# Kernel tuning notes

Measured on AMD Instinct MI355X. Metric: run time of the kernel, lower is better.

## Reference

```python
import jax, jax.numpy as jnp
import numpy as np

B, S, H = 4, 2048, 4096   # batch, seq, hidden
Q_DIM = 32 * 128          # num_attention_heads * head_dim
KV_DIM = 8 * 128          # num_key_value_heads * head_dim
R = 16                    # lora_r
SCALING = 32.0 / 16.0     # lora_alpha / lora_r


def setup_inputs() -> dict:
    key = jax.random.key(0)
    ks = jax.random.split(key, 10)
    def n(k, shape, scale):
        return jax.random.normal(k, shape, dtype=jnp.float32) * scale
    x = jax.random.normal(ks[0], (B, S, H), dtype=jnp.float32)
    # base weights stored as [out_dim, in_dim] like nn.Linear
    Wq = n(ks[1], (Q_DIM, H), 0.02)
    Wk = n(ks[2], (KV_DIM, H), 0.02)
    Wv = n(ks[3], (KV_DIM, H), 0.02)
    bq = n(ks[4], (Q_DIM,), 0.02)
    bk = n(ks[5], (KV_DIM,), 0.02)
    bv = n(ks[6], (KV_DIM,), 0.02)
    # LoRA A: kaiming-uniform-like init; B: zeros in training start, use small
    # random values here so the LoRA path is numerically exercised.
    bound = 1.0 / np.sqrt(H)
    Aq = jax.random.uniform(ks[7], (H, R), jnp.float32, -bound, bound)
    Ak = jax.random.uniform(ks[8], (H, R), jnp.float32, -bound, bound)
    Av = jax.random.uniform(ks[9], (H, R), jnp.float32, -bound, bound)
    kb = jax.random.split(jax.random.fold_in(key, 1), 3)
    Bq = n(kb[0], (R, Q_DIM), 0.01)
    Bk = n(kb[1], (R, KV_DIM), 0.01)
    Bv = n(kb[2], (R, KV_DIM), 0.01)
    return {"x": x, "Wq": Wq, "Wk": Wk, "Wv": Wv, "bq": bq, "bk": bk, "bv": bv,
            "Aq": Aq, "Bq": Bq, "Ak": Ak, "Bk": Bk, "Av": Av, "Bv": Bv}


def _proj(x, W, b, A, Bm):
    # base GEMM + low-rank LoRA delta + bias (dropout p=0 -> identity)
    base = jnp.einsum('bsh,oh->bso', x, W)
    delta = jnp.einsum('bsr,ro->bso', jnp.einsum('bsh,hr->bsr', x, A), Bm)
    return base + SCALING * delta + b


def reference(x, Wq, Wk, Wv, bq, bk, bv, Aq, Bq, Ak, Bk, Av, Bv):
    q = _proj(x, Wq, bq, Aq, Bq)  # [B,S,Q_DIM]
    k = _proj(x, Wk, bk, Ak, Bk)  # [B,S,KV_DIM]
    v = _proj(x, Wv, bv, Av, Bv)  # [B,S,KV_DIM]
    return q, k, v
```

## Files before the change

kernel.cpp:

```cpp
#include <hip/hip_runtime.h>


#define GLOBAL_AS __attribute__((address_space(1)))
#define LDS_AS    __attribute__((address_space(3)))

typedef __attribute__((ext_vector_type(8))) short  short8;
typedef __attribute__((ext_vector_type(4))) float  floatx4;

constexpr int Mdim = 8192;
constexpr int Kdim = 4096;
constexpr int NQ   = 4096;
constexpr int NKV  = 1024;
constexpr int NTOT = NQ + 2 * NKV;
constexpr float LORA_SCALE = 2.0f;

constexpr int BM = 256, BN = 256;
constexpr int TILES_M = Mdim / BM;
constexpr int TILES_N = NTOT / BN;
constexpr int NWG = TILES_M * TILES_N;
constexpr int NSLICE = Kdim / 32;

constexpr int WEFF_BLOCKS = (NTOT / 64) * (Kdim / 512);
constexpr int CVT_BLOCKS  = 2048;
constexpr int AT_STRIDE   = 516;

__device__ __forceinline__ unsigned short f2bf(float f) {
    union { float f; unsigned int u; } a; a.f = f;
    unsigned int r = a.u + 0x7FFFu + ((a.u >> 16) & 1u);
    return (unsigned short)(r >> 16);
}

__global__ __launch_bounds__(256)
void prep_kernel(const float4* __restrict__ x4, unsigned short* __restrict__ Xbf,
                 const float* __restrict__ Wq, const float* __restrict__ Wk,
                 const float* __restrict__ Wv,
                 const float* __restrict__ Aq, const float* __restrict__ Bq,
                 const float* __restrict__ Ak, const float* __restrict__ Bk,
                 const float* __restrict__ Av, const float* __restrict__ Bv,
                 unsigned short* __restrict__ Wf) {
    __shared__ float AsT[16 * AT_STRIDE];
    __shared__ float Bsc[64 * 16];

    const int tid = threadIdx.x;

    if (blockIdx.x >= WEFF_BLOCKS) {
        int i = (blockIdx.x - WEFF_BLOCKS) * 256 + tid;
        const int stride = CVT_BLOCKS * 256;
        const int n4 = Mdim * Kdim / 4;
        ushort4* out = (ushort4*)Xbf;
        for (; i < n4; i += stride) {
            float4 v = x4[i];
            ushort4 u;
            u.x = f2bf(v.x); u.y = f2bf(v.y); u.z = f2bf(v.z); u.w = f2bf(v.w);
            out[i] = u;
        }
        return;
    }

    const int n0 = (blockIdx.x >> 3) * 64;
    const int h0 = (blockIdx.x & 7) * 512;

    const float* W; const float* A; const float* Bm; int O; int nn0;
    if (n0 < NQ)            { W = Wq; A = Aq; Bm = Bq; O = NQ;  nn0 = n0; }
    else if (n0 < NQ + NKV) { W = Wk; A = Ak; Bm = Bk; O = NKV; nn0 = n0 - NQ; }
    else                    { W = Wv; A = Av; Bm = Bv; O = NKV; nn0 = n0 - NQ - NKV; }

    {
        const float4* Af4 = (const float4*)(A) + h0 * 4;
        #pragma unroll
        for (int i = 0; i < 8; ++i) {
            const int f = i * 256 + tid;
            const float4 v = Af4[f];
            const int hl = f >> 2;
            const int r0 = (f & 3) * 4;
            AsT[(r0 + 0) * AT_STRIDE + hl] = v.x;
            AsT[(r0 + 1) * AT_STRIDE + hl] = v.y;
            AsT[(r0 + 2) * AT_STRIDE + hl] = v.z;
            AsT[(r0 + 3) * AT_STRIDE + hl] = v.w;
        }
    }
    {
        const int nl = tid & 63;
        const int rq = tid >> 6;
        #pragma unroll
        for (int j = 0; j < 4; ++j) {
            const int r = rq * 4 + j;
            Bsc[nl * 16 + r] = Bm[r * O + nn0 + nl] * LORA_SCALE;
        }
    }
    __syncthreads();

    const int wv_ = tid >> 6;
    const int lane = tid & 63;

    #pragma unroll
    for (int pass = 0; pass < 2; ++pass) {
        const int hl = pass * 256 + lane * 4;
        float4 areg[16];
        #pragma unroll
        for (int r = 0; r < 16; ++r)
            areg[r] = *(const float4*)(&AsT[r * AT_STRIDE + hl]);

        for (int i = 0; i < 16; ++i) {
            const int nl = wv_ * 16 + i;
            const float4 w4 = *(const float4*)(W + (size_t)(nn0 + nl) * Kdim + h0 + hl);
            const float4* b4 = (const float4*)(&Bsc[nl * 16]);
            float4 d = {0.f, 0.f, 0.f, 0.f};
            #pragma unroll
            for (int q = 0; q < 4; ++q) {
                const float4 b = b4[q];
                d.x += areg[q*4+0].x * b.x + areg[q*4+1].x * b.y + areg[q*4+2].x * b.z + areg[q*4+3].x * b.w;
                d.y += areg[q*4+0].y * b.x + areg[q*4+1].y * b.y + areg[q*4+2].y * b.z + areg[q*4+3].y * b.w;
                d.z += areg[q*4+0].z * b.x + areg[q*4+1].z * b.y + areg[q*4+2].z * b.z + areg[q*4+3].z * b.w;
                d.w += areg[q*4+0].w * b.x + areg[q*4+1].w * b.y + areg[q*4+2].w * b.z + areg[q*4+3].w * b.w;
            }
            ushort4 u;
            u.x = f2bf(w4.x + d.x); u.y = f2bf(w4.y + d.y);
            u.z = f2bf(w4.z + d.z); u.w = f2bf(w4.w + d.w);
            *(ushort4*)(Wf + (size_t)(n0 + nl) * Kdim + h0 + hl) = u;
        }
    }
}

__global__ __launch_bounds__(512, 2)
void gemm_qkv_kernel(const unsigned short* __restrict__ X,
                     const unsigned short* __restrict__ Wf,
                     const float* __restrict__ bq, const float* __restrict__ bk,
                     const float* __restrict__ bv,
                     float* __restrict__ out) {
    __shared__ __align__(16) unsigned short Abuf[4][8192];
    __shared__ __align__(16) unsigned short Bbuf[4][8192];

    const int tid  = threadIdx.x;
    const int lane = tid & 63;
    const int w    = tid >> 6;
    const int wr   = w >> 2;
    const int wc   = w & 3;

    int bid = blockIdx.x;
    bid = (bid & 7) * (NWG / 8) + (bid >> 3);
    const int row0 = (bid / TILES_N) * BM;
    const int col0 = (bid % TILES_N) * BN;

    const int swz    = (((lane >> 4) ^ ((lane >> 1) & 3)) << 4);
    const int aByte0 = (wr * 128 + (lane & 15)) * 64 + swz;
    const int bByte0 = (wc * 64  + (lane & 15)) * 64 + swz;

    const int srow = (w << 4) + (lane >> 2);
    const int kswz = (((lane & 3) ^ ((lane >> 3) & 3)) << 3);
    const unsigned short* pA0 = X  + (size_t)(row0 + srow) * Kdim + kswz;
    const unsigned short* pA1 = pA0 + (size_t)128 * Kdim;
    const unsigned short* pB0 = Wf + (size_t)(col0 + srow) * Kdim + kswz;
    const unsigned short* pB1 = pB0 + (size_t)128 * Kdim;

    floatx4 acc[8][4];
    #pragma unroll
    for (int i = 0; i < 8; ++i)
        #pragma unroll
        for (int j = 0; j < 4; ++j)
            acc[i][j] = (floatx4){0.f, 0.f, 0.f, 0.f};

    short8 afr[2][4];
    short8 bfr[2][4];

#define STAGE(MATA, SS, SLOT)                                                    \
    { const int ss_ = (SS);                                                      \
      if (MATA) {                                                                \
        __builtin_amdgcn_global_load_lds((const GLOBAL_AS void*)(pA0 + ss_ * 32),\
            (LDS_AS void*)(&Abuf[SLOT][w * 512]),        16, 0, 0);              \
        __builtin_amdgcn_global_load_lds((const GLOBAL_AS void*)(pA1 + ss_ * 32),\
            (LDS_AS void*)(&Abuf[SLOT][4096 + w * 512]), 16, 0, 0);              \
      } else {                                                                   \
        __builtin_amdgcn_global_load_lds((const GLOBAL_AS void*)(pB0 + ss_ * 32),\
            (LDS_AS void*)(&Bbuf[SLOT][w * 512]),        16, 0, 0);              \
        __builtin_amdgcn_global_load_lds((const GLOBAL_AS void*)(pB1 + ss_ * 32),\
            (LDS_AS void*)(&Bbuf[SLOT][4096 + w * 512]), 16, 0, 0);              \
      } }

#define READA(P, SLOT, MH)                                                       \
    { const char* ab_ = (const char*)Abuf + (SLOT) * 16384;                      \
      _Pragma("unroll")                                                          \
      for (int mf = 0; mf < 4; ++mf)                                             \
        afr[P][mf] = *(const short8*)(ab_ + aByte0 + ((MH) * 4 + mf) * 1024); }

#define READB(P, SLOT)                                                           \
    { const char* bb_ = (const char*)Bbuf + (SLOT) * 16384;                      \
      _Pragma("unroll")                                                          \
      for (int nf = 0; nf < 4; ++nf)                                             \
        bfr[P][nf] = *(const short8*)(bb_ + bByte0 + nf * 1024); }

#define MFMA16(PA, PB, MH)                                                       \
    { __builtin_amdgcn_s_setprio(1);                                             \
      _Pragma("unroll")                                                          \
      for (int mf = 0; mf < 4; ++mf)                                             \
        _Pragma("unroll")                                                        \
        for (int nf = 0; nf < 4; ++nf)                                           \
          acc[(MH) * 4 + mf][nf] = __builtin_amdgcn_mfma_f32_16x16x32_bf16(      \
              afr[PA][mf], bfr[PB][nf], acc[(MH) * 4 + mf][nf], 0, 0, 0);        \
      __builtin_amdgcn_s_setprio(0); }

#define PHASE(PAC, PBC, MH, PRA, NAP, NSLOT, NMH, PRB, NBP, DOST, SM, SS, SSLOT, WM, BAR) \
    { if (PRA) READA(NAP, NSLOT, NMH);                                           \
      if (PRB) READB(NBP, NSLOT);                                                \
      if (DOST) STAGE(SM, SS, SSLOT);                                            \
      MFMA16(PAC, PBC, MH);                                                      \
      if ((WM) == 1) asm volatile("s_waitcnt vmcnt(6)" ::: "memory");            \
      if ((WM) == 2) asm volatile("s_waitcnt vmcnt(4)" ::: "memory");            \
      if ((WM) == 3) asm volatile("s_waitcnt vmcnt(0)" ::: "memory");            \
      if (BAR) __builtin_amdgcn_s_barrier(); }

    STAGE(1, 0, 0); STAGE(0, 0, 0);
    STAGE(1, 1, 1); STAGE(0, 1, 1);
    STAGE(1, 2, 2); STAGE(0, 2, 2);
    asm volatile("s_waitcnt vmcnt(8)" ::: "memory");
    __builtin_amdgcn_s_barrier();
    READA(0, 0, 0);
    READB(0, 0);

    for (int j = 0; j < NSLICE / 4 - 1; ++j) {
        const int g = j * 4;
        PHASE(0,  0,  0,  1,  1,  0,    1,  0,  0,   1,   1,  g + 3, 3,    1, 1);
        PHASE(1,  0,  1,  1,  0,  1,    0,  1,  1,   1,   0,  g + 3, 3,    0, 1);
        PHASE(0,  1,  0,  1,  1,  1,    1,  0,  0,   1,   1,  g + 4, 0,    1, 1);
        PHASE(1,  1,  1,  1,  0,  2,    0,  1,  0,   1,   0,  g + 4, 0,    0, 1);
        PHASE(0,  0,  0,  1,  1,  2,    1,  0,  0,   1,   1,  g + 5, 1,    1, 1);
        PHASE(1,  0,  1,  1,  0,  3,    0,  1,  1,   1,   0,  g + 5, 1,    0, 1);
        PHASE(0,  1,  0,  1,  1,  3,    1,  0,  0,   1,   1,  g + 6, 2,    1, 1);
        PHASE(1,  1,  1,  1,  0,  0,    0,  1,  0,   1,   0,  g + 6, 2,    0, 1);
    }
    PHASE(0, 0, 0,  1, 1, 0, 1,  0, 0,  1, 1, 127, 3,  1, 1);
    PHASE(1, 0, 1,  1, 0, 1, 0,  1, 1,  1, 0, 127, 3,  0, 1);
    PHASE(0, 1, 0,  1, 1, 1, 1,  0, 0,  0, 0, 0,   0,  2, 1);
    PHASE(1, 1, 1,  1, 0, 2, 0,  1, 0,  0, 0, 0,   0,  0, 1);
    PHASE(0, 0, 0,  1, 1, 2, 1,  0, 0,  0, 0, 0,   0,  3, 1);
    PHASE(1, 0, 1,  1, 0, 3, 0,  1, 1,  0, 0, 0,   0,  0, 1);
    PHASE(0, 1, 0,  1, 1, 3, 1,  0, 0,  0, 0, 0,   0,  0, 1);
    PHASE(1, 1, 1,  0, 0, 0, 0,  0, 0,  0, 0, 0,   0,  0, 0);

#undef PHASE
#undef MFMA16
#undef READB
#undef READA
#undef STAGE

    float* obase; int ldo; const float* bias; int cofs;
    if (col0 < NQ) {
        obase = out;                             ldo = NQ;  bias = bq; cofs = 0;
    } else if (col0 < NQ + NKV) {
        obase = out + (size_t)Mdim * NQ;         ldo = NKV; bias = bk; cofs = NQ;
    } else {
        obase = out + (size_t)Mdim * (NQ + NKV); ldo = NKV; bias = bv; cofs = NQ + NKV;
    }

    #pragma unroll
    for (int nf = 0; nf < 4; ++nf) {
        const int col = col0 + wc * 64 + nf * 16 + (lane & 15) - cofs;
        const float b = bias[col];
        #pragma unroll
        for (int mf = 0; mf < 8; ++mf) {
            #pragma unroll
            for (int r = 0; r < 4; ++r) {
                const int row = row0 + wr * 128 + mf * 16 + (lane >> 4) * 4 + r;
                obase[(size_t)row * ldo + col] = acc[mf][nf][r] + b;
            }
        }
    }
}

extern "C" void kernel_launch(void* const* d_in, const int* in_sizes, int n_in,
                              void* d_out, int out_size, void* d_ws, size_t ws_size,
                              hipStream_t stream) {
    const float* x  = (const float*)d_in[0];
    const float* Wq = (const float*)d_in[1];
    const float* Wk = (const float*)d_in[2];
    const float* Wv = (const float*)d_in[3];
    const float* bq = (const float*)d_in[4];
    const float* bk = (const float*)d_in[5];
    const float* bv = (const float*)d_in[6];
    const float* Aq = (const float*)d_in[7];
    const float* Bq = (const float*)d_in[8];
    const float* Ak = (const float*)d_in[9];
    const float* Bk = (const float*)d_in[10];
    const float* Av = (const float*)d_in[11];
    const float* Bv = (const float*)d_in[12];
    float* out = (float*)d_out;

    unsigned short* Xbf = (unsigned short*)d_ws;
    unsigned short* Wf  = Xbf + (size_t)Mdim * Kdim;

    prep_kernel<<<WEFF_BLOCKS + CVT_BLOCKS, 256, 0, stream>>>(
        (const float4*)x, Xbf, Wq, Wk, Wv, Aq, Bq, Ak, Bk, Av, Bv, Wf);

    gemm_qkv_kernel<<<NWG, 512, 0, stream>>>(Xbf, Wf, bq, bk, bv, out);
}
```

Baseline: 472.9 us.

## Restructure GEMM main loop into per-slice phases with unswizzled LDS layout

```diff
diff --git a/kernel.cpp b/kernel.cpp
--- a/kernel.cpp
+++ b/kernel.cpp
@@ -142,15 +142,15 @@
     const int row0 = (bid / TILES_N) * BM;
     const int col0 = (bid % TILES_N) * BN;
 
-    const int swz    = (((lane >> 4) ^ ((lane >> 1) & 3)) << 4);
-    const int aByte0 = (wr * 128 + (lane & 15)) * 64 + swz;
-    const int bByte0 = (wc * 64  + (lane & 15)) * 64 + swz;
-
-    const int srow = (w << 4) + (lane >> 2);
-    const int kswz = (((lane & 3) ^ ((lane >> 3) & 3)) << 3);
-    const unsigned short* pA0 = X  + (size_t)(row0 + srow) * Kdim + kswz;
+    const int lane16 = lane * 16;
+    const int aBase0 = wr * 8192 + lane16;
+    const int bBase0 = (wc >> 1) * 8192 + (wc & 1) * 4096 + lane16;
+
+    const int srow = w * 16 + (lane & 15);
+    const int kofs = (lane >> 4) * 8;
+    const unsigned short* pA0 = X  + (size_t)(row0 + srow) * Kdim + kofs;
     const unsigned short* pA1 = pA0 + (size_t)128 * Kdim;
-    const unsigned short* pB0 = Wf + (size_t)(col0 + srow) * Kdim + kswz;
+    const unsigned short* pB0 = Wf + (size_t)(col0 + srow) * Kdim + kofs;
     const unsigned short* pB1 = pB0 + (size_t)128 * Kdim;
 
     floatx4 acc[8][4];
@@ -160,88 +160,63 @@
         for (int j = 0; j < 4; ++j)
             acc[i][j] = (floatx4){0.f, 0.f, 0.f, 0.f};
 
-    short8 afr[2][4];
-    short8 bfr[2][4];
-
-#define STAGE(MATA, SS, SLOT)                                                    \
+#define STAGE4(SS, SLOT)                                                         \
     { const int ss_ = (SS);                                                      \
-      if (MATA) {                                                                \
-        __builtin_amdgcn_global_load_lds((const GLOBAL_AS void*)(pA0 + ss_ * 32),\
-            (LDS_AS void*)(&Abuf[SLOT][w * 512]),        16, 0, 0);              \
-        __builtin_amdgcn_global_load_lds((const GLOBAL_AS void*)(pA1 + ss_ * 32),\
-            (LDS_AS void*)(&Abuf[SLOT][4096 + w * 512]), 16, 0, 0);              \
-      } else {                                                                   \
-        __builtin_amdgcn_global_load_lds((const GLOBAL_AS void*)(pB0 + ss_ * 32),\
-            (LDS_AS void*)(&Bbuf[SLOT][w * 512]),        16, 0, 0);              \
-        __builtin_amdgcn_global_load_lds((const GLOBAL_AS void*)(pB1 + ss_ * 32),\
-            (LDS_AS void*)(&Bbuf[SLOT][4096 + w * 512]), 16, 0, 0);              \
-      } }
-
-#define READA(P, SLOT, MH)                                                       \
-    { const char* ab_ = (const char*)Abuf + (SLOT) * 16384;                      \
+      __builtin_amdgcn_global_load_lds((const GLOBAL_AS void*)(pA0 + ss_ * 32),  \
+          (LDS_AS void*)(&Abuf[SLOT][w * 512]),        16, 0, 0);                \
+      __builtin_amdgcn_global_load_lds((const GLOBAL_AS void*)(pA1 + ss_ * 32),  \
+          (LDS_AS void*)(&Abuf[SLOT][4096 + w * 512]), 16, 0, 0);                \
+      __builtin_amdgcn_global_load_lds((const GLOBAL_AS void*)(pB0 + ss_ * 32),  \
+          (LDS_AS void*)(&Bbuf[SLOT][w * 512]),        16, 0, 0);                \
+      __builtin_amdgcn_global_load_lds((const GLOBAL_AS void*)(pB1 + ss_ * 32),  \
+          (LDS_AS void*)(&Bbuf[SLOT][4096 + w * 512]), 16, 0, 0); }
+
+#define SLICE_PHASE(SLOT, DOSTAGE, SS, WM)                                       \
+    { const char* ab_ = (const char*)Abuf + (SLOT) * 16384 + aBase0;             \
+      const char* bb_ = (const char*)Bbuf + (SLOT) * 16384 + bBase0;             \
+      short8 af[8]; short8 bfr[4];                                               \
       _Pragma("unroll")                                                          \
-      for (int mf = 0; mf < 4; ++mf)                                             \
-        afr[P][mf] = *(const short8*)(ab_ + aByte0 + ((MH) * 4 + mf) * 1024); }
-
-#define READB(P, SLOT)                                                           \
-    { const char* bb_ = (const char*)Bbuf + (SLOT) * 16384;                      \
+      for (int mf = 0; mf < 8; ++mf)                                             \
+        af[mf] = *(const short8*)(ab_ + mf * 1024);                              \
       _Pragma("unroll")                                                          \
       for (int nf = 0; nf < 4; ++nf)                                             \
-        bfr[P][nf] = *(const short8*)(bb_ + bByte0 + nf * 1024); }
-
-#define MFMA16(PA, PB, MH)                                                       \
-    { __builtin_amdgcn_s_setprio(1);                                             \
+        bfr[nf] = *(const short8*)(bb_ + nf * 1024);                             \
+      if (DOSTAGE) STAGE4(SS, (SS) & 3);                                         \
+      __builtin_amdgcn_s_barrier();                                              \
+      asm volatile("s_waitcnt lgkmcnt(0)");                                      \
+      __builtin_amdgcn_s_setprio(1);                                             \
       _Pragma("unroll")                                                          \
-      for (int mf = 0; mf < 4; ++mf)                                             \
+      for (int mf = 0; mf < 8; ++mf)                                             \
         _Pragma("unroll")                                                        \
         for (int nf = 0; nf < 4; ++nf)                                           \
-          acc[(MH) * 4 + mf][nf] = __builtin_amdgcn_mfma_f32_16x16x32_bf16(      \
-              afr[PA][mf], bfr[PB][nf], acc[(MH) * 4 + mf][nf], 0, 0, 0);        \
-      __builtin_amdgcn_s_setprio(0); }
-
-#define PHASE(PAC, PBC, MH, PRA, NAP, NSLOT, NMH, PRB, NBP, DOST, SM, SS, SSLOT, WM, BAR) \
-    { if (PRA) READA(NAP, NSLOT, NMH);                                           \
-      if (PRB) READB(NBP, NSLOT);                                                \
-      if (DOST) STAGE(SM, SS, SSLOT);                                            \
-      MFMA16(PAC, PBC, MH);                                                      \
-      if ((WM) == 1) asm volatile("s_waitcnt vmcnt(6)" ::: "memory");            \
+          acc[mf][nf] = __builtin_amdgcn_mfma_f32_16x16x32_bf16(                 \
+              af[mf], bfr[nf], acc[mf][nf], 0, 0, 0);                            \
+      __builtin_amdgcn_s_setprio(0);                                             \
+      if ((WM) == 1) asm volatile("s_waitcnt vmcnt(8)" ::: "memory");            \
       if ((WM) == 2) asm volatile("s_waitcnt vmcnt(4)" ::: "memory");            \
       if ((WM) == 3) asm volatile("s_waitcnt vmcnt(0)" ::: "memory");            \
-      if (BAR) __builtin_amdgcn_s_barrier(); }
-
-    STAGE(1, 0, 0); STAGE(0, 0, 0);
-    STAGE(1, 1, 1); STAGE(0, 1, 1);
-    STAGE(1, 2, 2); STAGE(0, 2, 2);
+      __builtin_amdgcn_s_barrier(); }
+
+    STAGE4(0, 0);
+    STAGE4(1, 1);
+    STAGE4(2, 2);
     asm volatile("s_waitcnt vmcnt(8)" ::: "memory");
     __builtin_amdgcn_s_barrier();
-    READA(0, 0, 0);
-    READB(0, 0);
-
-    for (int j = 0; j < NSLICE / 4 - 1; ++j) {
+
+    for (int j = 0; j < 31; ++j) {
         const int g = j * 4;
-        PHASE(0,  0,  0,  1,  1,  0,    1,  0,  0,   1,   1,  g + 3, 3,    1, 1);
-        PHASE(1,  0,  1,  1,  0,  1,    0,  1,  1,   1,   0,  g + 3, 3,    0, 1);
-        PHASE(0,  1,  0,  1,  1,  1,    1,  0,  0,   1,   1,  g + 4, 0,    1, 1);
-        PHASE(1,  1,  1,  1,  0,  2,    0,  1,  0,   1,   0,  g + 4, 0,    0, 1);
-        PHASE(0,  0,  0,  1,  1,  2,    1,  0,  0,   1,   1,  g + 5, 1,    1, 1);
-        PHASE(1,  0,  1,  1,  0,  3,    0,  1,  1,   1,   0,  g + 5, 1,    0, 1);
-        PHASE(0,  1,  0,  1,  1,  3,    1,  0,  0,   1,   1,  g + 6, 2,    1, 1);
-        PHASE(1,  1,  1,  1,  0,  0,    0,  1,  0,   1,   0,  g + 6, 2,    0, 1);
-    }
-    PHASE(0, 0, 0,  1, 1, 0, 1,  0, 0,  1, 1, 127, 3,  1, 1);
-    PHASE(1, 0, 1,  1, 0, 1, 0,  1, 1,  1, 0, 127, 3,  0, 1);
-    PHASE(0, 1, 0,  1, 1, 1, 1,  0, 0,  0, 0, 0,   0,  2, 1);
-    PHASE(1, 1, 1,  1, 0, 2, 0,  1, 0,  0, 0, 0,   0,  0, 1);
-    PHASE(0, 0, 0,  1, 1, 2, 1,  0, 0,  0, 0, 0,   0,  3, 1);
-    PHASE(1, 0, 1,  1, 0, 3, 0,  1, 1,  0, 0, 0,   0,  0, 1);
-    PHASE(0, 1, 0,  1, 1, 3, 1,  0, 0,  0, 0, 0,   0,  0, 1);
-    PHASE(1, 1, 1,  0, 0, 0, 0,  0, 0,  0, 0, 0,   0,  0, 0);
-
-#undef PHASE
-#undef MFMA16
-#undef READB
-#undef READA
-#undef STAGE
+        SLICE_PHASE(0, 1, g + 3, 1);
+        SLICE_PHASE(1, 1, g + 4, 1);
+        SLICE_PHASE(2, 1, g + 5, 1);
+        SLICE_PHASE(3, 1, g + 6, 1);
+    }
+    SLICE_PHASE(0, 1, 127, 1);
+    SLICE_PHASE(1, 0, 0,   2);
+    SLICE_PHASE(2, 0, 0,   3);
+    SLICE_PHASE(3, 0, 0,   0);
+
+#undef SLICE_PHASE
+#undef STAGE4
 
     float* obase; int ldo; const float* bias; int cofs;
     if (col0 < NQ) {
```

New measurement: 577.4 us. 22.1% more time.
